# Kernel optimization log

Hardware: AMD Instinct MI355X
Metric: run time of the kernel (lower is better)

The kernel has to match this reference:

```python
import jax, jax.numpy as jnp
import numpy as np

N_GROUP = 8
TOPK_GROUP = 4
TOP_K = 8
ROUTED_SCALE = 2.5


def setup_inputs() -> dict:
    key = jax.random.key(0)
    ks = jax.random.split(key, 8)
    B, S, D, E, I = 4, 2048, 2048, 32, 1024
    s = 0.02
    return {
        "x": jax.random.normal(ks[0], (B, S, D), jnp.float32),
        "gate_w": jax.random.normal(ks[1], (D, E), jnp.float32) * s,
        "e_bias": jnp.zeros((E,), jnp.float32),
        "gate_up": jax.random.normal(ks[2], (E, D, 2 * I), jnp.float32) * s,
        "down": jax.random.normal(ks[3], (E, I, D), jnp.float32) * s,
        "shared_gate": jax.random.normal(ks[4], (D, I), jnp.float32) * s,
        "shared_up": jax.random.normal(ks[5], (D, I), jnp.float32) * s,
        "shared_down": jax.random.normal(ks[6], (I, D), jnp.float32) * s,
    }


def _router(x_flat, gate_w, e_bias):
    N, E = x_flat.shape[0], gate_w.shape[1]
    epg = E // N_GROUP  # experts per group
    logits = x_flat @ gate_w                                   # [N, E]
    scores = jax.nn.sigmoid(logits.astype(jnp.float32))        # [N, E]
    sfr = scores + e_bias                                      # routing scores
    grouped = sfr.reshape(N, N_GROUP, epg)
    group_scores = jax.lax.top_k(grouped, min(2, epg))[0].sum(-1)   # [N, G]
    topk_group_idx = jax.lax.top_k(group_scores, TOPK_GROUP)[1]     # [N, topk_group]
    group_mask = jnp.zeros((N, N_GROUP), bool).at[
        jnp.arange(N)[:, None], topk_group_idx].set(True)
    expert_mask = jnp.repeat(group_mask, epg, axis=1)          # [N, E]
    masked = jnp.where(expert_mask, sfr, -jnp.inf)
    topk_idx = jax.lax.top_k(masked, TOP_K)[1]                 # [N, K]
    topk_w = jnp.take_along_axis(scores, topk_idx, axis=1)     # [N, K]
    topk_w = topk_w / (topk_w.sum(-1, keepdims=True) + 1e-20)  # norm_topk_prob
    topk_w = topk_w * ROUTED_SCALE
    return topk_idx, topk_w, scores


def _experts(x_flat, topk_idx, topk_w, gate_up, down):
    N, D = x_flat.shape
    E, K = gate_up.shape[0], topk_idx.shape[1]
    flat = topk_idx.reshape(-1)                                # [N*K]
    sort_idx = jnp.argsort(flat)                               # route: group rows by expert
    sorted_tokens = x_flat[sort_idx // K]                      # [N*K, D]
    group_sizes = jnp.bincount(flat, length=E).astype(jnp.int32)
    h = jax.lax.ragged_dot(sorted_tokens, gate_up, group_sizes)  # [N*K, 2I]
    gate_h, up_h = jnp.split(h, 2, axis=-1)
    inter = jax.nn.silu(gate_h) * up_h                         # SwiGLU
    out = jax.lax.ragged_dot(inter, down, group_sizes)         # [N*K, D]
    unsorted = jnp.zeros_like(out).at[sort_idx].set(out)       # unroute
    return (unsorted.reshape(N, K, D) * topk_w[..., None].astype(out.dtype)).sum(1)


def _shared_mlp(x, wg, wu, wd):
    return (jax.nn.silu(x @ wg) * (x @ wu)) @ wd


def reference(x, gate_w, e_bias, gate_up, down, shared_gate, shared_up, shared_down):
    B, S, D = x.shape
    x_flat = x.reshape(B * S, D)
    topk_idx, topk_w, scores = _router(x_flat, gate_w, e_bias)
    routed = _experts(x_flat, topk_idx, topk_w, gate_up, down).reshape(B, S, D)
    output = routed + _shared_mlp(x, shared_gate, shared_up, shared_down)
    return output, topk_idx, scores
```

## Files before the change

### kernel.cpp

```cpp
#include <hip/hip_runtime.h>
#include <hip/hip_bf16.h>
#include <math.h>


typedef __bf16 bf16_t;
typedef __bf16 bf16x8 __attribute__((ext_vector_type(8)));
typedef float  f32x4  __attribute__((ext_vector_type(4)));

constexpr int NTOK = 8192;
constexpr int D    = 2048;
constexpr int E    = 32;
constexpr int I    = 1024;
constexpr int TK   = 8;
constexpr int NK   = NTOK * TK;
constexpr int TM   = 256;
constexpr int MAX_TILES = E + NK / TM;
constexpr float RSCALE = 2.5f;

#define GL16(g, l) __builtin_amdgcn_global_load_lds( \
    (const __attribute__((address_space(1))) void*)(g), \
    (__attribute__((address_space(3))) void*)(l), 16, 0, 0)


__global__ __launch_bounds__(64) void k_zero_meta(int* counts, int* cursors, int* ntl) {
    int t = threadIdx.x;
    if (t < E) { counts[t] = 0; cursors[t] = 0; }
    if (t == 0) *ntl = 0;
}

__global__ __launch_bounds__(64) void k_sentinel(float* out) {
    if (threadIdx.x == 0) out[0] = 12345.0f;
}

__global__ __launch_bounds__(256) void k_convert_x(const float* __restrict__ src,
                                                   bf16_t* __restrict__ dst, int n8) {
    int i = blockIdx.x * 256 + threadIdx.x;
    if (i >= n8) return;
    const float4* s = (const float4*)src;
    float4 a = s[(size_t)i * 2], b = s[(size_t)i * 2 + 1];
    bf16_t t[8] = {(bf16_t)a.x, (bf16_t)a.y, (bf16_t)a.z, (bf16_t)a.w,
                   (bf16_t)b.x, (bf16_t)b.y, (bf16_t)b.z, (bf16_t)b.w};
    *(uint4*)(dst + (size_t)i * 8) = *(const uint4*)t;
}

template <int MODE>
__global__ __launch_bounds__(256) void k_transpose(const float* __restrict__ src,
                                                   bf16_t* __restrict__ dst,
                                                   int R, int C,
                                                   size_t srcMat, size_t dstMat) {
    __shared__ float t[32][33];
    int b = blockIdx.z;
    const float* s = src + (size_t)b * srcMat;
    bf16_t* d = dst + (size_t)b * dstMat;
    int c0 = blockIdx.x * 32, r0 = blockIdx.y * 32;
    int tx = threadIdx.x, ty = threadIdx.y;
#pragma unroll
    for (int yy = 0; yy < 4; yy++)
        t[ty + yy * 8][tx] = s[(size_t)(r0 + ty + yy * 8) * C + c0 + tx];
    __syncthreads();
#pragma unroll
    for (int yy = 0; yy < 4; yy++) {
        int c = c0 + ty + yy * 8;
        int rc = (MODE == 0) ? c
               : (MODE == 1) ? ((c < I) ? 2 * c : 2 * (c - I) + 1)
               : (MODE == 2) ? 2 * c : 2 * c + 1;
        d[(size_t)rc * R + r0 + tx] = (bf16_t)t[tx][ty + yy * 8];
    }
}


__global__ __launch_bounds__(256) void k_router(const float* __restrict__ x,
                                                const float* __restrict__ gw,
                                                const float* __restrict__ eb,
                                                float* __restrict__ out_idx,
                                                float* __restrict__ out_scores,
                                                float* __restrict__ topk_w,
                                                int* __restrict__ tok_expert,
                                                int* __restrict__ counts) {
    int t = blockIdx.x;
    int tid = threadIdx.x;
    int e = tid & 31, part = tid >> 5;
    const float* xr = x + (size_t)t * D;
    float partial = 0.f;
    int d0 = part * 256;
    for (int d = d0; d < d0 + 256; d++)
        partial += xr[d] * gw[(size_t)d * E + e];

    __shared__ float red[8][32];
    __shared__ float sc[32], sfr[32];
    red[part][e] = partial;
    __syncthreads();
    if (tid < 32) {
        float l = 0.f;
#pragma unroll
        for (int p = 0; p < 8; p++) l += red[p][tid];
        float s = 1.f / (1.f + expf(-l));
        sc[tid] = s;
        sfr[tid] = s + eb[tid];
        out_scores[(size_t)t * E + tid] = s;
    }
    __syncthreads();
    if (tid == 0) {
        float gs[8];
#pragma unroll
        for (int g = 0; g < 8; g++) {
            float m1 = -1e30f, m2 = -1e30f;
#pragma unroll
            for (int i = 0; i < 4; i++) {
                float v = sfr[g * 4 + i];
                if (v > m1) { m2 = m1; m1 = v; } else if (v > m2) m2 = v;
            }
            gs[g] = m1 + m2;
        }
        bool gsel[8] = {false, false, false, false, false, false, false, false};
        for (int it = 0; it < 4; it++) {
            int bi = -1; float bv = -1e30f;
            for (int g = 0; g < 8; g++)
                if (!gsel[g] && gs[g] > bv) { bv = gs[g]; bi = g; }
            gsel[bi] = true;
        }
        float masked[32];
        for (int i = 0; i < 32; i++) masked[i] = gsel[i >> 2] ? sfr[i] : -1e30f;
        int idx[TK]; float w[TK]; float wsum = 0.f;
        for (int k = 0; k < TK; k++) {
            int bi = 0; float bv = -1e30f;
            for (int i = 0; i < 32; i++)
                if (masked[i] > bv) { bv = masked[i]; bi = i; }
            masked[bi] = -1e30f;
            idx[k] = bi; w[k] = sc[bi]; wsum += w[k];
        }
        float inv = RSCALE / (wsum + 1e-20f);
        for (int k = 0; k < TK; k++) {
            out_idx[(size_t)t * TK + k] = (float)idx[k];
            topk_w[(size_t)t * TK + k] = w[k] * inv;
            tok_expert[(size_t)t * TK + k] = idx[k];
            atomicAdd(&counts[idx[k]], 1);
        }
    }
}

__global__ __launch_bounds__(64) void k_offsets(const int* __restrict__ counts,
                                                int* __restrict__ offs,
                                                int4* __restrict__ ttbl,
                                                int* __restrict__ ntl) {
    if (threadIdx.x != 0) return;
    int off = 0, nt = 0;
    for (int e = 0; e < E; e++) {
        offs[e] = off;
        int c = counts[e];
        for (int r = 0; r < c; r += TM) {
            ttbl[nt] = make_int4(off + r, min(TM, c - r), e, 0);
            nt++;
        }
        off += c;
    }
    offs[E] = off;
    *ntl = nt;
}

__global__ __launch_bounds__(256) void k_scatter(const int* __restrict__ tok_expert,
                                                 const int* __restrict__ offs,
                                                 int* __restrict__ cursors,
                                                 int* __restrict__ slot_token,
                                                 int* __restrict__ slot_inv) {
    int i = blockIdx.x * 256 + threadIdx.x;
    if (i >= NK) return;
    int e = tok_expert[i];
    int pos = offs[e] + atomicAdd(&cursors[e], 1);
    slot_token[pos] = i >> 3;
    slot_inv[i] = pos;
}


#define SCB() __builtin_amdgcn_sched_barrier(0)

#define PEND() do { asm volatile("s_waitcnt vmcnt(4)" ::: "memory"); \
    __builtin_amdgcn_s_barrier(); SCB(); } while (0)

#define SA2(b, rnd, k0) do { \
    GL16(gA[0][rnd] + (k0), smb + (b) * 65536 + (rnd) * 8192 + w * 1024); \
    GL16(gA[1][rnd] + (k0), smb + (b) * 65536 + 16384 + (rnd) * 8192 + w * 1024); } while (0)

#define SB(b, h, k0) do { \
    GL16(gB[h][0] + (k0), smb + (b) * 65536 + 32768 + (h) * 16384 + w * 1024); \
    GL16(gB[h][1] + (k0), smb + (b) * 65536 + 32768 + (h) * 16384 + 8192 + w * 1024); } while (0)

#define LDA(b, mh) do { _Pragma("unroll") for (int m_ = 0; m_ < 4; m_++) { \
    aF[m_][0] = *(const bf16x8*)(smb + (b) * 65536 + wm * 16384 + (mh) * 8192 + m_ * 2048 + lofs0); \
    aF[m_][1] = *(const bf16x8*)(smb + (b) * 65536 + wm * 16384 + (mh) * 8192 + m_ * 2048 + lofs1); } } while (0)

#define LDB(dst, b, nh) do { _Pragma("unroll") for (int n_ = 0; n_ < 2; n_++) { \
    dst[n_][0] = *(const bf16x8*)(smb + (b) * 65536 + 32768 + wn * 8192 + (nh) * 4096 + n_ * 2048 + lofs0); \
    dst[n_][1] = *(const bf16x8*)(smb + (b) * 65536 + 32768 + wn * 8192 + (nh) * 4096 + n_ * 2048 + lofs1); } } while (0)

#define MMA(bv, MH, NH) do { \
    __builtin_amdgcn_s_setprio(1); \
    _Pragma("unroll") for (int m_ = 0; m_ < 4; m_++) \
    _Pragma("unroll") for (int n_ = 0; n_ < 2; n_++) { \
    acc[(MH) * 4 + m_][(NH) * 2 + n_] = __builtin_amdgcn_mfma_f32_16x16x32_bf16( \
        aF[m_][0], bv[n_][0], acc[(MH) * 4 + m_][(NH) * 2 + n_], 0, 0, 0); \
    acc[(MH) * 4 + m_][(NH) * 2 + n_] = __builtin_amdgcn_mfma_f32_16x16x32_bf16( \
        aF[m_][1], bv[n_][1], acc[(MH) * 4 + m_][(NH) * 2 + n_], 0, 0, 0); } \
    __builtin_amdgcn_s_setprio(0); } while (0)

template <bool EXPERT, bool GATHER, int EPI>
__global__ __launch_bounds__(512, 2) void k_mm8(const bf16_t* __restrict__ A,
                                                const bf16_t* __restrict__ Bt,
                                                int K, size_t estride,
                                                const int* __restrict__ slot_token,
                                                const int4* __restrict__ ttbl,
                                                const int* __restrict__ ntl,
                                                void* __restrict__ C, int ldc) {
    int L = (int)blockIdx.y * 8 + (int)blockIdx.x;
    int xcd = L & 7, k = L >> 3;
    int per = (int)gridDim.y >> 3;
    int ty = xcd * per + (k >> 3);
    int tx = k & 7;

    int base_slot, rows, e;
    if (EXPERT) {
        if (ty >= *ntl) return;
        int4 tt = ttbl[ty];
        base_slot = tt.x; rows = tt.y; e = tt.z;
    } else {
        base_slot = ty * TM; rows = TM; e = 0;
    }
    int c0 = tx * 256;
    const bf16_t* Bw = Bt + (size_t)e * estride + (size_t)c0 * K;

    extern __shared__ char smb[];

    int tid = threadIdx.x, lane = tid & 63, w = tid >> 6;
    int wm = w >> 2, wn = w & 3;
    int lr = lane & 15, hi = lane >> 4;
    int rx = lr & 7;
    int lofs0 = lr * 128 + ((hi ^ rx) << 4);
    int lofs1 = lr * 128 + (((4 + hi) ^ rx) << 4);

    int srow = tid >> 3;
    int cbg = (tid & 7) ^ (srow & 7);
    const bf16_t* gA[2][2]; const bf16_t* gB[2][2];
#pragma unroll
    for (int h = 0; h < 2; h++)
#pragma unroll
        for (int rnd = 0; rnd < 2; rnd++) {
            int r = h * 128 + rnd * 64 + srow;
            int ar = min(r, rows - 1);
            int tok = GATHER ? slot_token[base_slot + ar] : (base_slot + ar);
            gA[h][rnd] = A + (size_t)tok * K + cbg * 8;
            gB[h][rnd] = Bw + (size_t)r * K + cbg * 8;
        }

    f32x4 acc[8][4] = {};
    bf16x8 aF[4][2], b0[2][2], b1[2][2];

    SA2(0, 0, 0); SA2(0, 1, 0);
    SB(0, 0, 0); SB(0, 1, 0);
    SA2(1, 0, 64);
    SB(1, 0, 64); SB(1, 1, 64);
    asm volatile("s_waitcnt vmcnt(0)" ::: "memory");
    __builtin_amdgcn_s_barrier();
    SCB();
    LDA(0, 0); LDB(b0, 0, 0);

    int nt = K >> 6;
    for (int kt = 0; kt < nt; kt += 2) {
        int k1 = (kt + 1) << 6;
        int k2 = (kt + 2 < nt) ? (kt + 2) << 6 : 0;
        int k3 = (kt + 3 < nt) ? (kt + 3) << 6 : 0;
        LDB(b1, 0, 1);
        MMA(b0, 0, 0);
        SA2(1, 1, k1);
        PEND();
        MMA(b1, 0, 1);
        LDA(0, 1);
        SA2(0, 0, k2);
        PEND();
        MMA(b0, 1, 0);
        SB(0, 0, k2);
        PEND();
        MMA(b1, 1, 1);
        LDA(1, 0); LDB(b0, 1, 0);
        SB(0, 1, k2);
        PEND();
        LDB(b1, 1, 1);
        MMA(b0, 0, 0);
        SA2(0, 1, k2);
        PEND();
        MMA(b1, 0, 1);
        LDA(1, 1);
        SA2(1, 0, k3);
        PEND();
        MMA(b0, 1, 0);
        SB(1, 0, k3);
        PEND();
        MMA(b1, 1, 1);
        LDA(0, 0); LDB(b0, 0, 0);
        SB(1, 1, k3);
        PEND();
    }

#pragma unroll
    for (int mi = 0; mi < 8; mi++) {
#pragma unroll
        for (int j = 0; j < 4; j++) {
            int r = wm * 128 + mi * 16 + hi * 4 + j;
            bool valid = !EXPERT || (r < rows);
            size_t orow = (size_t)base_slot + r;
#pragma unroll
            for (int f = 0; f < 4; f++) {
                float v = acc[mi][f][j];
                int c = c0 + wn * 64 + f * 16 + lr;
                if (EPI == 0) {
                    float o = __shfl_xor(v, 1);
                    float g = (lane & 1) ? o : v;
                    float u = (lane & 1) ? v : o;
                    float sv = g / (1.f + __expf(-g)) * u;
                    if (valid && !(lane & 1))
                        ((bf16_t*)C)[orow * ldc + (c >> 1)] = (bf16_t)sv;
                } else if (EPI == 1) {
                    float o = __shfl_xor(v, 1);
                    if (valid && !(lane & 1)) {
                        bf16_t pr[2] = {(bf16_t)v, (bf16_t)o};
                        *(unsigned int*)((bf16_t*)C + orow * ldc + c) = *(unsigned int*)pr;
                    }
                } else {
                    if (valid) ((float*)C)[orow * ldc + c] = v;
                }
            }
        }
    }
}


__global__ __launch_bounds__(256) void k_finalize(const bf16_t* __restrict__ outS,
                                                  const int* __restrict__ slot_inv,
                                                  const float* __restrict__ tkw,
                                                  float* __restrict__ out) {
    int tok = blockIdx.x, tid = threadIdx.x;
    __shared__ int sp[TK];
    __shared__ float swt[TK];
    if (tid < TK) {
        sp[tid] = slot_inv[tok * TK + tid];
        swt[tid] = tkw[tok * TK + tid];
    }
    __syncthreads();
    int c = tid * 8;
    float* op = out + (size_t)tok * D + c;
    float acc[8];
    float4 o0 = *(float4*)op, o1 = *(float4*)(op + 4);
    acc[0] = o0.x; acc[1] = o0.y; acc[2] = o0.z; acc[3] = o0.w;
    acc[4] = o1.x; acc[5] = o1.y; acc[6] = o1.z; acc[7] = o1.w;
#pragma unroll
    for (int k = 0; k < TK; k++) {
        bf16x8 v = *(const bf16x8*)(outS + (size_t)sp[k] * D + c);
        float w = swt[k];
#pragma unroll
        for (int j = 0; j < 8; j++) acc[j] += w * (float)v[j];
    }
    o0 = make_float4(acc[0], acc[1], acc[2], acc[3]);
    o1 = make_float4(acc[4], acc[5], acc[6], acc[7]);
    *(float4*)op = o0;
    *(float4*)(op + 4) = o1;
}


extern "C" void kernel_launch(void* const* d_in, const int* in_sizes, int n_in,
                              void* d_out, int out_size, void* d_ws, size_t ws_size,
                              hipStream_t stream) {
    const float* x  = (const float*)d_in[0];
    const float* gw = (const float*)d_in[1];
    const float* eb = (const float*)d_in[2];
    const float* gu = (const float*)d_in[3];
    const float* dn = (const float*)d_in[4];
    const float* sg = (const float*)d_in[5];
    const float* su = (const float*)d_in[6];
    const float* sd = (const float*)d_in[7];

    float* out        = (float*)d_out;
    float* out_idx    = out + (size_t)NTOK * D;
    float* out_scores = out_idx + (size_t)NTOK * TK;

    char* w = (char*)d_ws;
    auto alloc = [&](size_t bytes) {
        char* p = w;
        w += (bytes + 255) & ~(size_t)255;
        return p;
    };
    bf16_t* xb      = (bf16_t*)alloc((size_t)NTOK * D * 2);
    bf16_t* gut     = (bf16_t*)alloc((size_t)E * 2 * I * D * 2);
    bf16_t* dnt     = (bf16_t*)alloc((size_t)E * D * I * 2);
    bf16_t* sh1t    = (bf16_t*)alloc((size_t)2 * I * D * 2);
    bf16_t* sdt     = (bf16_t*)alloc((size_t)D * I * 2);
    bf16_t* inter   = (bf16_t*)alloc((size_t)NK * I * 2);
    bf16_t* inter_s = (bf16_t*)alloc((size_t)NTOK * I * 2);
    float*  tkw     = (float*)alloc((size_t)NK * 4);
    int*    tke     = (int*)alloc((size_t)NK * 4);
    int*    stok    = (int*)alloc((size_t)NK * 4);
    int*    sinv    = (int*)alloc((size_t)NK * 4);
    int*    counts  = (int*)alloc(E * 4);
    int*    offs    = (int*)alloc((E + 1) * 4);
    int*    curs    = (int*)alloc(E * 4);
    int4*   ttbl    = (int4*)alloc(MAX_TILES * 16);
    int*    ntl     = (int*)alloc(4);
    bf16_t* outS    = gut;

    if ((size_t)(w - (char*)d_ws) > ws_size) {
        k_sentinel<<<1, 64, 0, stream>>>(out);
        return;
    }

    k_zero_meta<<<1, 64, 0, stream>>>(counts, curs, ntl);
    k_convert_x<<<(NTOK * D / 8 + 255) / 256, 256, 0, stream>>>(x, xb, NTOK * D / 8);

    k_transpose<1><<<dim3(2 * I / 32, D / 32, E), dim3(32, 8), 0, stream>>>(
        gu, gut, D, 2 * I, (size_t)D * 2 * I, (size_t)D * 2 * I);
    k_transpose<0><<<dim3(D / 32, I / 32, E), dim3(32, 8), 0, stream>>>(
        dn, dnt, I, D, (size_t)I * D, (size_t)I * D);
    k_transpose<2><<<dim3(I / 32, D / 32, 1), dim3(32, 8), 0, stream>>>(
        sg, sh1t, D, I, 0, 0);
    k_transpose<3><<<dim3(I / 32, D / 32, 1), dim3(32, 8), 0, stream>>>(
        su, sh1t, D, I, 0, 0);
    k_transpose<0><<<dim3(D / 32, I / 32, 1), dim3(32, 8), 0, stream>>>(
        sd, sdt, I, D, 0, 0);

    k_router<<<NTOK, 256, 0, stream>>>(x, gw, eb, out_idx, out_scores, tkw, tke, counts);
    k_offsets<<<1, 64, 0, stream>>>(counts, offs, ttbl, ntl);
    k_scatter<<<NK / 256, 256, 0, stream>>>(tke, offs, curs, stok, sinv);

    constexpr size_t SMEM = 131072;
    k_mm8<true, true, 0><<<dim3(8, MAX_TILES), 512, SMEM, stream>>>(
        xb, gut, D, (size_t)2 * I * D, stok, ttbl, ntl, inter, I);
    k_mm8<true, false, 1><<<dim3(8, MAX_TILES), 512, SMEM, stream>>>(
        inter, dnt, I, (size_t)D * I, stok, ttbl, ntl, outS, D);

    k_mm8<false, false, 0><<<dim3(8, NTOK / TM), 512, SMEM, stream>>>(
        xb, sh1t, D, 0, nullptr, nullptr, nullptr, inter_s, I);
    k_mm8<false, false, 2><<<dim3(8, NTOK / TM), 512, SMEM, stream>>>(
        inter_s, sdt, I, 0, nullptr, nullptr, nullptr, out, D);

    k_finalize<<<NTOK, 256, 0, stream>>>(outS, sinv, tkw, out);
}
```

Measured before the change: 1.821 ms.

## Double-buffer A fragments and issue LDS reads before MFMA blocks in GEMM loop

Reworks the main GEMM loop so that each phase issues its LDS fragment loads and global-to-LDS prefetches before the MFMA block, separated by a sched barrier. A fragments get even/odd register double buffers, like the B fragments, so the loads can overlap the preceding MFMAs. B global pointers are collapsed into one base pointer with computed row offsets, which saves address registers. The extra fragment registers could raise register pressure under launch_bounds(512,2), and the reordered LDS reads relative to the barriers need careful hazard correctness.

```diff
diff --git a/kernel.cpp b/kernel.cpp
--- a/kernel.cpp
+++ b/kernel.cpp
@@ -182,25 +182,25 @@
     GL16(gA[1][rnd] + (k0), smb + (b) * 65536 + 16384 + (rnd) * 8192 + w * 1024); } while (0)
 
 #define SB(b, h, k0) do { \
-    GL16(gB[h][0] + (k0), smb + (b) * 65536 + 32768 + (h) * 16384 + w * 1024); \
-    GL16(gB[h][1] + (k0), smb + (b) * 65536 + 32768 + (h) * 16384 + 8192 + w * 1024); } while (0)
-
-#define LDA(b, mh) do { _Pragma("unroll") for (int m_ = 0; m_ < 4; m_++) { \
-    aF[m_][0] = *(const bf16x8*)(smb + (b) * 65536 + wm * 16384 + (mh) * 8192 + m_ * 2048 + lofs0); \
-    aF[m_][1] = *(const bf16x8*)(smb + (b) * 65536 + wm * 16384 + (mh) * 8192 + m_ * 2048 + lofs1); } } while (0)
+    GL16(gBb + (size_t)((h) * 128) * K + (k0), smb + (b) * 65536 + 32768 + (h) * 16384 + w * 1024); \
+    GL16(gBb + (size_t)((h) * 128 + 64) * K + (k0), smb + (b) * 65536 + 32768 + (h) * 16384 + 8192 + w * 1024); } while (0)
+
+#define LDA(dst, b, mh) do { _Pragma("unroll") for (int m_ = 0; m_ < 4; m_++) { \
+    dst[m_][0] = *(const bf16x8*)(smb + (b) * 65536 + wm * 16384 + (mh) * 8192 + m_ * 2048 + lofs0); \
+    dst[m_][1] = *(const bf16x8*)(smb + (b) * 65536 + wm * 16384 + (mh) * 8192 + m_ * 2048 + lofs1); } } while (0)
 
 #define LDB(dst, b, nh) do { _Pragma("unroll") for (int n_ = 0; n_ < 2; n_++) { \
     dst[n_][0] = *(const bf16x8*)(smb + (b) * 65536 + 32768 + wn * 8192 + (nh) * 4096 + n_ * 2048 + lofs0); \
     dst[n_][1] = *(const bf16x8*)(smb + (b) * 65536 + 32768 + wn * 8192 + (nh) * 4096 + n_ * 2048 + lofs1); } } while (0)
 
-#define MMA(bv, MH, NH) do { \
+#define MMA(av, bv, MH, NH) do { \
     __builtin_amdgcn_s_setprio(1); \
     _Pragma("unroll") for (int m_ = 0; m_ < 4; m_++) \
     _Pragma("unroll") for (int n_ = 0; n_ < 2; n_++) { \
     acc[(MH) * 4 + m_][(NH) * 2 + n_] = __builtin_amdgcn_mfma_f32_16x16x32_bf16( \
-        aF[m_][0], bv[n_][0], acc[(MH) * 4 + m_][(NH) * 2 + n_], 0, 0, 0); \
+        av[m_][0], bv[n_][0], acc[(MH) * 4 + m_][(NH) * 2 + n_], 0, 0, 0); \
     acc[(MH) * 4 + m_][(NH) * 2 + n_] = __builtin_amdgcn_mfma_f32_16x16x32_bf16( \
-        aF[m_][1], bv[n_][1], acc[(MH) * 4 + m_][(NH) * 2 + n_], 0, 0, 0); } \
+        av[m_][1], bv[n_][1], acc[(MH) * 4 + m_][(NH) * 2 + n_], 0, 0, 0); } \
     __builtin_amdgcn_s_setprio(0); } while (0)
 
 template <bool EXPERT, bool GATHER, int EPI>
@@ -239,7 +239,7 @@
 
     int srow = tid >> 3;
     int cbg = (tid & 7) ^ (srow & 7);
-    const bf16_t* gA[2][2]; const bf16_t* gB[2][2];
+    const bf16_t* gA[2][2];
 #pragma unroll
     for (int h = 0; h < 2; h++)
 #pragma unroll
@@ -248,11 +248,11 @@
             int ar = min(r, rows - 1);
             int tok = GATHER ? slot_token[base_slot + ar] : (base_slot + ar);
             gA[h][rnd] = A + (size_t)tok * K + cbg * 8;
-            gB[h][rnd] = Bw + (size_t)r * K + cbg * 8;
-        }
+        }
+    const bf16_t* gBb = Bw + (size_t)srow * K + cbg * 8;
 
     f32x4 acc[8][4] = {};
-    bf16x8 aF[4][2], b0[2][2], b1[2][2];
+    bf16x8 aE[4][2], aO[4][2], bE[2][2], bO[2][2];
 
     SA2(0, 0, 0); SA2(0, 1, 0);
     SB(0, 0, 0); SB(0, 1, 0);
@@ -261,43 +261,29 @@
     asm volatile("s_waitcnt vmcnt(0)" ::: "memory");
     __builtin_amdgcn_s_barrier();
     SCB();
-    LDA(0, 0); LDB(b0, 0, 0);
+    LDA(aE, 0, 0); LDB(bE, 0, 0);
 
     int nt = K >> 6;
     for (int kt = 0; kt < nt; kt += 2) {
         int k1 = (kt + 1) << 6;
         int k2 = (kt + 2 < nt) ? (kt + 2) << 6 : 0;
         int k3 = (kt + 3 < nt) ? (kt + 3) << 6 : 0;
-        LDB(b1, 0, 1);
-        MMA(b0, 0, 0);
-        SA2(1, 1, k1);
-        PEND();
-        MMA(b1, 0, 1);
-        LDA(0, 1);
-        SA2(0, 0, k2);
-        PEND();
-        MMA(b0, 1, 0);
-        SB(0, 0, k2);
-        PEND();
-        MMA(b1, 1, 1);
-        LDA(1, 0); LDB(b0, 1, 0);
-        SB(0, 1, k2);
-        PEND();
-        LDB(b1, 1, 1);
-        MMA(b0, 0, 0);
-        SA2(0, 1, k2);
-        PEND();
-        MMA(b1, 0, 1);
-        LDA(1, 1);
-        SA2(1, 0, k3);
-        PEND();
-        MMA(b0, 1, 0);
-        SB(1, 0, k3);
-        PEND();
-        MMA(b1, 1, 1);
-        LDA(0, 0); LDB(b0, 0, 0);
-        SB(1, 1, k3);
-        PEND();
+        LDB(bO, 0, 1); SA2(1, 1, k1); SCB();
+        MMA(aE, bE, 0, 0); PEND();
+        LDA(aO, 0, 1); SA2(0, 0, k2); SCB();
+        MMA(aE, bO, 0, 1); PEND();
+        LDA(aE, 1, 0); SB(0, 0, k2); SCB();
+        MMA(aO, bE, 1, 0); PEND();
+        LDB(bE, 1, 0); SB(0, 1, k2); SCB();
+        MMA(aO, bO, 1, 1); PEND();
+        LDB(bO, 1, 1); SA2(0, 1, k2); SCB();
+        MMA(aE, bE, 0, 0); PEND();
+        LDA(aO, 1, 1); SA2(1, 0, k3); SCB();
+        MMA(aE, bO, 0, 1); PEND();
+        LDA(aE, 0, 0); SB(1, 0, k3); SCB();
+        MMA(aO, bE, 1, 0); PEND();
+        LDB(bE, 0, 0); SB(1, 1, k3); SCB();
+        MMA(aO, bO, 1, 1); PEND();
     }
 
 #pragma unroll
```

After: 2.762 ms. 51.7% more time.
